# Performance work log

Measured on AMD Instinct MI355X. Metric: run time of the kernel, lower is better.

The kernel has to match this reference:

```python
import jax, jax.numpy as jnp
import numpy as np

EPS = 1e-5

def _layernorm(x, g, b):
    m = jnp.mean(x, axis=-1, keepdims=True)
    v = jnp.mean((x - m) ** 2, axis=-1, keepdims=True)
    return (x - m) * jax.lax.rsqrt(v + EPS) * g + b

def setup_inputs() -> dict:
    key = jax.random.key(0)
    ks = jax.random.split(key, 16)
    B, N, L, E, D, NL = 1, 40962, 256, 4, 163848, 6
    inp = {}
    inp['mesh_latent'] = jax.random.normal(ks[0], (B, N, L), dtype=jnp.float32)
    inp['edge_index'] = jax.random.randint(ks[1], (2, D), 0, N, dtype=jnp.int32)
    inp['edge_attr'] = jax.random.normal(ks[2], (D, E), dtype=jnp.float32)
    s_e = 1.0 / np.sqrt(2 * L + E)
    s_n = 1.0 / np.sqrt(2 * L)
    s_o = 1.0 / np.sqrt(L)
    inp['We_w'] = jax.random.uniform(ks[3], (NL, 2 * L + E, L), jnp.float32, -s_e, s_e)
    inp['We_b'] = jax.random.uniform(ks[4], (NL, L), jnp.float32, -s_e, s_e)
    inp['ln1_g'] = jnp.ones((NL, L), jnp.float32)
    inp['ln1_b'] = jnp.zeros((NL, L), jnp.float32)
    inp['Wn1_w'] = jax.random.uniform(ks[5], (NL, 2 * L, L), jnp.float32, -s_n, s_n)
    inp['Wn1_b'] = jax.random.uniform(ks[6], (NL, L), jnp.float32, -s_n, s_n)
    inp['ln2_g'] = jnp.ones((NL, L), jnp.float32)
    inp['ln2_b'] = jnp.zeros((NL, L), jnp.float32)
    inp['Wn2_w'] = jax.random.uniform(ks[7], (NL, L, L), jnp.float32, -s_o, s_o)
    inp['Wn2_b'] = jax.random.uniform(ks[8], (NL, L), jnp.float32, -s_o, s_o)
    return inp

def reference(mesh_latent, edge_index, edge_attr, We_w, We_b, ln1_g, ln1_b,
              Wn1_w, Wn1_b, ln2_g, ln2_b, Wn2_w, Wn2_b):
    src = edge_index[0]  # x_j (source)
    dst = edge_index[1]  # x_i (target), also aggregation index
    N = mesh_latent.shape[1]
    L = mesh_latent.shape[2]
    # precompute edge_attr contribution is layer-dependent, done inside scan

    def layer(x, p):
        we_w, we_b, g1, b1, wn1_w, wn1_b, g2, b2, wn2_w, wn2_b = p
        x_i = x[dst]  # [E, L] target node feats
        x_j = x[src]  # [E, L] source node feats
        # edge MLP on cat([x_i, x_j, edge_attr]) without materializing the concat
        h = x_i @ we_w[:L] + x_j @ we_w[L:2 * L] + edge_attr @ we_w[2 * L:] + we_b
        msg = jax.nn.silu(_layernorm(h, g1, b1))  # [E, L]
        agg = jax.ops.segment_sum(msg, dst, num_segments=N)  # [N, L]
        u = x @ wn1_w[:L] + agg @ wn1_w[L:] + wn1_b
        u = jax.nn.silu(_layernorm(u, g2, b2)) @ wn2_w + wn2_b
        return x + u, None

    params = (We_w, We_b, ln1_g, ln1_b, Wn1_w, Wn1_b, ln2_g, ln2_b, Wn2_w, Wn2_b)

    def per_sample(x):
        x_out, _ = jax.lax.scan(layer, x, params)
        return x_out

    return jax.vmap(per_sample)(mesh_latent)
```

## Files before the change

### kernel.cpp

```cpp
#include <hip/hip_runtime.h>
#include <hip/hip_bf16.h>
#include <math.h>


#define NNODES 40962
#define NEDGES 163848
#define NLAYERS 6

typedef __attribute__((ext_vector_type(8))) short short8;
typedef __attribute__((ext_vector_type(4))) float f32x4;

__device__ __forceinline__ void async_copy16(void* lds, const void* g) {
    __builtin_amdgcn_global_load_lds(
        (const __attribute__((address_space(1))) unsigned int*)g,
        (__attribute__((address_space(3))) unsigned int*)lds, 16, 0, 0);
}

__global__ __launch_bounds__(256) void wprep_kernel(
    const float* __restrict__ src, unsigned short* __restrict__ dst,
    int R, int C, size_t src_lstride, size_t src_hstride, int halves)
{
    __shared__ float t[32][33];
    const int b = blockIdx.z;
    src += (size_t)(b / halves) * src_lstride + (size_t)(b % halves) * src_hstride;
    dst += (size_t)b * R * C;
    const int tx = threadIdx.x & 31, ty = threadIdx.x >> 5;
    const int c0 = blockIdx.x * 32, r0 = blockIdx.y * 32;
    #pragma unroll
    for (int i = 0; i < 4; ++i)
        t[ty + 8 * i][tx] = src[(size_t)(r0 + ty + 8 * i) * C + c0 + tx];
    __syncthreads();
    #pragma unroll
    for (int i = 0; i < 4; ++i) {
        unsigned int u = __float_as_uint(t[tx][ty + 8 * i]);
        unsigned short h = (unsigned short)((u + 0x7FFFu + ((u >> 16) & 1u)) >> 16);
        dst[(size_t)(c0 + ty + 8 * i) * R + r0 + tx] = h;
    }
}

__global__ __launch_bounds__(256) void gemm_mfma(
    const float* __restrict__ A1, const float* __restrict__ A2,
    const unsigned short* __restrict__ BT,
    const float* __restrict__ bias, const float* __restrict__ resid,
    float* __restrict__ C, int M, int K, int ldC)
{
    __shared__ __align__(16) short Ah[128 * 40];
    __shared__ __align__(16) short Al[128 * 40];
    __shared__ __align__(16) short Bs[128 * 32];

    const int tid = threadIdx.x;
    const int wave = tid >> 6;
    const int lane = tid & 63;
    const int m0 = blockIdx.x * 128;
    const int n0 = blockIdx.y * 128;
    const int wm = wave >> 1;
    const int wn = wave & 1;
    const int fm = lane & 15;
    const int quad = lane >> 4;
    const int ko = quad * 8;

    const int arow = tid >> 1;
    const int akh = (tid & 1) * 16;
    const int gr_stage = m0 + arow;

    f32x4 acc[4][4];
    #pragma unroll
    for (int i = 0; i < 4; ++i)
        #pragma unroll
        for (int j = 0; j < 4; ++j)
            acc[i][j] = (f32x4){0.f, 0.f, 0.f, 0.f};

    const int nkt = K >> 5;
    for (int kt = 0; kt < nkt; ++kt) {
        const int k0 = kt << 5;
        const float* Asrc; int kb;
        if (A2 != nullptr && k0 >= 256) { Asrc = A2; kb = k0 - 256; }
        else                            { Asrc = A1; kb = k0; }

        {
            const int n_row = wave * 32 + (lane >> 2);
            const char* gbase = (const char*)BT + (((size_t)(n0 + n_row) * K + k0) << 1)
                              + ((lane & 3) << 4);
            char* lbase = (char*)Bs + wave * 2048;
            async_copy16(lbase, gbase);
            const char* gbase2 = gbase + ((size_t)16 * K << 1);
            async_copy16(lbase + 1024, gbase2);
        }

        {
            float f[16];
            if (gr_stage < M) {
                const float* ap = Asrc + (size_t)gr_stage * 256 + kb + akh;
                #pragma unroll
                for (int i = 0; i < 4; ++i) {
                    f32x4 v = *(const f32x4*)(ap + 4 * i);
                    f[4 * i + 0] = v.x; f[4 * i + 1] = v.y;
                    f[4 * i + 2] = v.z; f[4 * i + 3] = v.w;
                }
            } else {
                #pragma unroll
                for (int i = 0; i < 16; ++i) f[i] = 0.f;
            }
            unsigned int hid[8], lod[8];
            #pragma unroll
            for (int i = 0; i < 8; ++i) {
                unsigned int u0 = __float_as_uint(f[2 * i]);
                unsigned int u1 = __float_as_uint(f[2 * i + 1]);
                float l0 = f[2 * i]     - __uint_as_float(u0 & 0xFFFF0000u);
                float l1 = f[2 * i + 1] - __uint_as_float(u1 & 0xFFFF0000u);
                hid[i] = (u0 >> 16) | (u1 & 0xFFFF0000u);
                lod[i] = (__float_as_uint(l0) >> 16) | (__float_as_uint(l1) & 0xFFFF0000u);
            }
            short* ah = &Ah[arow * 40 + akh];
            short* al = &Al[arow * 40 + akh];
            ((uint4*)ah)[0] = make_uint4(hid[0], hid[1], hid[2], hid[3]);
            ((uint4*)ah)[1] = make_uint4(hid[4], hid[5], hid[6], hid[7]);
            ((uint4*)al)[0] = make_uint4(lod[0], lod[1], lod[2], lod[3]);
            ((uint4*)al)[1] = make_uint4(lod[4], lod[5], lod[6], lod[7]);
        }

        __syncthreads();

        short8 afh[4], afl[4], bf[4];
        #pragma unroll
        for (int i = 0; i < 4; ++i) {
            const int r = wm * 64 + i * 16 + fm;
            afh[i] = *(const short8*)&Ah[r * 40 + ko];
            afl[i] = *(const short8*)&Al[r * 40 + ko];
        }
        #pragma unroll
        for (int j = 0; j < 4; ++j) {
            const int r = wn * 64 + j * 16 + fm;
            bf[j] = *(const short8*)&Bs[r * 32 + ko];
        }
        #pragma unroll
        for (int i = 0; i < 4; ++i)
            #pragma unroll
            for (int j = 0; j < 4; ++j) {
                acc[i][j] = __builtin_amdgcn_mfma_f32_16x16x32_bf16(afl[i], bf[j], acc[i][j], 0, 0, 0);
                acc[i][j] = __builtin_amdgcn_mfma_f32_16x16x32_bf16(afh[i], bf[j], acc[i][j], 0, 0, 0);
            }

        __syncthreads();
    }

    #pragma unroll
    for (int j = 0; j < 4; ++j) {
        const int gc = n0 + wn * 64 + j * 16 + fm;
        const float bj = bias ? bias[gc] : 0.f;
        #pragma unroll
        for (int i = 0; i < 4; ++i) {
            #pragma unroll
            for (int r = 0; r < 4; ++r) {
                const int gr = m0 + wm * 64 + i * 16 + quad * 4 + r;
                if (gr < M) {
                    float v = acc[i][j][r] + bj;
                    if (resid) v += resid[(size_t)gr * ldC + gc];
                    C[(size_t)gr * ldC + gc] = v;
                }
            }
        }
    }
}

__device__ __forceinline__ float wave_sum(float v) {
    #pragma unroll
    for (int o = 32; o > 0; o >>= 1) v += __shfl_xor(v, o);
    return v;
}

__global__ __launch_bounds__(256) void count_kernel(
    const int* __restrict__ dst, int* __restrict__ deg, int E)
{
    int e = blockIdx.x * 256 + threadIdx.x;
    if (e < E) atomicAdd(&deg[dst[e]], 1);
}

__global__ __launch_bounds__(1024) void scan_kernel(
    const int* __restrict__ deg, int* __restrict__ rowptr, int n)
{
    __shared__ int wsum[16];
    __shared__ int carry_s;
    const int tid = threadIdx.x;
    const int lane = tid & 63, wave = tid >> 6;
    if (tid == 0) carry_s = 0;
    __syncthreads();

    for (int base = 0; base < n; base += 1024) {
        int i = base + tid;
        int v = (i < n) ? deg[i] : 0;
        int x = v;
        #pragma unroll
        for (int o = 1; o < 64; o <<= 1) {
            int t = __shfl_up(x, o);
            if (lane >= o) x += t;
        }
        if (lane == 63) wsum[wave] = x;
        __syncthreads();
        if (wave == 0 && lane < 16) {
            int w = wsum[lane];
            #pragma unroll
            for (int o = 1; o < 16; o <<= 1) {
                int t = __shfl_up(w, o);
                if (lane >= o) w += t;
            }
            wsum[lane] = w;
        }
        __syncthreads();
        int wave_off = (wave == 0) ? 0 : wsum[wave - 1];
        int incl = x + wave_off + carry_s;
        if (i < n) rowptr[i] = incl - v;
        __syncthreads();
        if (tid == 0) carry_s += wsum[15];
        __syncthreads();
    }
    if (tid == 0) rowptr[n] = carry_s;
}

__global__ __launch_bounds__(256) void scatter_kernel(
    const int* __restrict__ dst, int* __restrict__ cursor,
    int* __restrict__ esorted, int E)
{
    int e = blockIdx.x * 256 + threadIdx.x;
    if (e < E) {
        int p = atomicAdd(&cursor[dst[e]], 1);
        esorted[p] = e;
    }
}

__global__ __launch_bounds__(256) void node_agg_kernel(
    const float* __restrict__ P,
    const int* __restrict__ src,
    const float* __restrict__ attr,
    const float* __restrict__ W3,
    const float* __restrict__ be, const float* __restrict__ g1, const float* __restrict__ b1,
    const int* __restrict__ rowptr, const int* __restrict__ esorted,
    float* __restrict__ agg, int N)
{
    const int wave = threadIdx.x >> 6;
    const int lane = threadIdx.x & 63;
    const int n = blockIdx.x * 4 + wave;
    if (n >= N) return;
    const int c0 = lane * 4;

    float4 p1 = *(const float4*)(P + (size_t)n * 512 + c0);
    const float* p1p = (const float*)&p1;

    float w30[4], w31[4], w32[4], w33[4], bev[4], g1v[4], b1v[4];
    #pragma unroll
    for (int i = 0; i < 4; ++i) {
        const int c = c0 + i;
        w30[i] = W3[c]; w31[i] = W3[256 + c]; w32[i] = W3[512 + c]; w33[i] = W3[768 + c];
        bev[i] = be[c]; g1v[i] = g1[c]; b1v[i] = b1[c];
    }

    float acc[4] = {0.f, 0.f, 0.f, 0.f};
    const int beg = rowptr[n];
    const int end = rowptr[n + 1];

    for (int i = beg; i < end; ++i) {
        const int e = esorted[i];
        const int s = src[e];
        float4 ps = *(const float4*)(P + (size_t)s * 512 + 256 + c0);
        const float* psp = (const float*)&ps;
        float4 av = *(const float4*)(attr + (size_t)e * 4);

        float h[4];
        #pragma unroll
        for (int j = 0; j < 4; ++j) {
            float w = av.x * w30[j] + av.y * w31[j] + av.z * w32[j] + av.w * w33[j];
            h[j] = p1p[j] + psp[j] + w + bev[j];
        }

        float sum = wave_sum(h[0] + h[1] + h[2] + h[3]);
        const float mean = sum * (1.0f / 256.0f);
        float vs = 0.f;
        #pragma unroll
        for (int j = 0; j < 4; ++j) { float t = h[j] - mean; vs += t * t; }
        vs = wave_sum(vs);
        const float rstd = rsqrtf(vs * (1.0f / 256.0f) + 1e-5f);

        #pragma unroll
        for (int j = 0; j < 4; ++j) {
            float y = (h[j] - mean) * rstd * g1v[j] + b1v[j];
            acc[j] += y / (1.0f + __expf(-y));
        }
    }

    *(float4*)(agg + (size_t)n * 256 + c0) = make_float4(acc[0], acc[1], acc[2], acc[3]);
}

__global__ __launch_bounds__(256) void ln_silu_kernel(
    float* __restrict__ u, const float* __restrict__ g, const float* __restrict__ b, int N)
{
    const int wave = threadIdx.x >> 6;
    const int lane = threadIdx.x & 63;
    const int r = blockIdx.x * 4 + wave;
    if (r >= N) return;

    float4 hv = *(const float4*)(u + (size_t)r * 256 + lane * 4);
    float h[4] = {hv.x, hv.y, hv.z, hv.w};

    float sum = wave_sum(h[0] + h[1] + h[2] + h[3]);
    const float mean = sum * (1.0f / 256.0f);
    float vs = 0.f;
    #pragma unroll
    for (int i = 0; i < 4; ++i) { float t = h[i] - mean; vs += t * t; }
    vs = wave_sum(vs);
    const float rstd = rsqrtf(vs * (1.0f / 256.0f) + 1e-5f);

    #pragma unroll
    for (int i = 0; i < 4; ++i) {
        const int c = lane * 4 + i;
        float y = (h[i] - mean) * rstd * g[c] + b[c];
        h[i] = y / (1.0f + __expf(-y));
    }
    *(float4*)(u + (size_t)r * 256 + lane * 4) = make_float4(h[0], h[1], h[2], h[3]);
}

extern "C" void kernel_launch(void* const* d_in, const int* in_sizes, int n_in,
                              void* d_out, int out_size, void* d_ws, size_t ws_size,
                              hipStream_t stream) {
    const float* mesh   = (const float*)d_in[0];
    const int*   eidx   = (const int*)  d_in[1];
    const float* eattr  = (const float*)d_in[2];
    const float* We_w   = (const float*)d_in[3];
    const float* We_b   = (const float*)d_in[4];
    const float* ln1_g  = (const float*)d_in[5];
    const float* ln1_b  = (const float*)d_in[6];
    const float* Wn1_w  = (const float*)d_in[7];
    const float* Wn1_b  = (const float*)d_in[8];
    const float* ln2_g  = (const float*)d_in[9];
    const float* ln2_b  = (const float*)d_in[10];
    const float* Wn2_w  = (const float*)d_in[11];
    const float* Wn2_b  = (const float*)d_in[12];

    const int N = NNODES, E = NEDGES;

    float* x   = (float*)d_out;
    float* P   = (float*)d_ws;
    float* u   = P;
    float* agg = P + (size_t)N * 512;
    int*   deg     = (int*)(agg + (size_t)N * 256);
    int*   rowptr  = deg + N;
    int*   cursor  = rowptr + (N + 1);
    int*   esorted = cursor + N;
    uintptr_t wp = (uintptr_t)(esorted + E);
    wp = (wp + 63) & ~(uintptr_t)63;
    unsigned short* BTe  = (unsigned short*)wp;
    unsigned short* BTn1 = BTe  + (size_t)6 * 512 * 256;
    unsigned short* BTn2 = BTn1 + (size_t)6 * 256 * 512;

    const int* src = eidx;
    const int* dst = eidx + E;

    hipMemcpyAsync(x, mesh, (size_t)N * 256 * sizeof(float),
                   hipMemcpyDeviceToDevice, stream);

    wprep_kernel<<<dim3(8, 8, 12), 256, 0, stream>>>(
        We_w, BTe, 256, 256, (size_t)516 * 256, (size_t)256 * 256, 2);
    wprep_kernel<<<dim3(8, 16, 6), 256, 0, stream>>>(
        Wn1_w, BTn1, 512, 256, (size_t)512 * 256, 0, 1);
    wprep_kernel<<<dim3(8, 8, 6), 256, 0, stream>>>(
        Wn2_w, BTn2, 256, 256, (size_t)256 * 256, 0, 1);

    hipMemsetAsync(deg, 0, (size_t)N * sizeof(int), stream);
    count_kernel<<<(E + 255) / 256, 256, 0, stream>>>(dst, deg, E);
    scan_kernel<<<1, 1024, 0, stream>>>(deg, rowptr, N);
    hipMemcpyAsync(cursor, rowptr, (size_t)N * sizeof(int),
                   hipMemcpyDeviceToDevice, stream);
    scatter_kernel<<<(E + 255) / 256, 256, 0, stream>>>(dst, cursor, esorted, E);

    const int mblocks = (N + 127) / 128;
    const int node_blocks = (N + 3) / 4;

    for (int l = 0; l < NLAYERS; ++l) {
        const float* W3  = We_w + (size_t)l * 516 * 256 + (size_t)512 * 256;
        const float* be  = We_b  + (size_t)l * 256;
        const float* g1  = ln1_g + (size_t)l * 256;
        const float* b1  = ln1_b + (size_t)l * 256;
        const float* bn1 = Wn1_b + (size_t)l * 256;
        const float* g2  = ln2_g + (size_t)l * 256;
        const float* b2  = ln2_b + (size_t)l * 256;
        const float* bn2 = Wn2_b + (size_t)l * 256;
        const unsigned short* bte  = BTe  + (size_t)l * 512 * 256;
        const unsigned short* btn1 = BTn1 + (size_t)l * 256 * 512;
        const unsigned short* btn2 = BTn2 + (size_t)l * 256 * 256;

        gemm_mfma<<<dim3(mblocks, 4), 256, 0, stream>>>(
            x, nullptr, bte, nullptr, nullptr, P, N, 256, 512);
        node_agg_kernel<<<node_blocks, 256, 0, stream>>>(
            P, src, eattr, W3, be, g1, b1, rowptr, esorted, agg, N);
        gemm_mfma<<<dim3(mblocks, 2), 256, 0, stream>>>(
            x, agg, btn1, bn1, nullptr, u, N, 512, 256);
        ln_silu_kernel<<<node_blocks, 256, 0, stream>>>(u, g2, b2, N);
        gemm_mfma<<<dim3(mblocks, 2), 256, 0, stream>>>(
            u, nullptr, btn2, bn2, x, x, N, 256, 256);
    }
}
```

Before: 1.519 ms.

## Pre-split activations to bf16 hi/lo in producers and async-load A tiles

Producers (split kernel, node aggregation, LN-SiLU, and the residual GEMM epilogue) now write activations as separate bf16 high and low halves. The GEMM can then stream A tiles with global_load_lds through an XOR-swizzled LDS layout instead of loading fp32 and converting in registers. Rows are padded to a multiple of 128 with zeroed tails so no bounds checks are needed. Node aggregation also processes two edges per iteration with prefetching, and both LayerNorms use a single-pass sum and sum-of-squares reduction, which risks some precision loss.

```diff
diff --git a/kernel.cpp b/kernel.cpp
--- a/kernel.cpp
+++ b/kernel.cpp
@@ -6,9 +6,11 @@
 #define NNODES 40962
 #define NEDGES 163848
 #define NLAYERS 6
+#define MPAD 41088
 
 typedef __attribute__((ext_vector_type(8))) short short8;
 typedef __attribute__((ext_vector_type(4))) float f32x4;
+typedef unsigned short ushort_t;
 
 __device__ __forceinline__ void async_copy16(void* lds, const void* g) {
     __builtin_amdgcn_global_load_lds(
@@ -16,8 +18,15 @@
         (__attribute__((address_space(3))) unsigned int*)lds, 16, 0, 0);
 }
 
+__device__ __forceinline__ void bsplit(float v, ushort_t& h, ushort_t& l) {
+    unsigned int u = __float_as_uint(v);
+    h = (ushort_t)(u >> 16);
+    float hf = __uint_as_float(u & 0xFFFF0000u);
+    l = (ushort_t)(__float_as_uint(v - hf) >> 16);
+}
+
 __global__ __launch_bounds__(256) void wprep_kernel(
-    const float* __restrict__ src, unsigned short* __restrict__ dst,
+    const float* __restrict__ src, ushort_t* __restrict__ dst,
     int R, int C, size_t src_lstride, size_t src_hstride, int halves)
 {
     __shared__ float t[32][33];
@@ -33,35 +42,54 @@
     #pragma unroll
     for (int i = 0; i < 4; ++i) {
         unsigned int u = __float_as_uint(t[tx][ty + 8 * i]);
-        unsigned short h = (unsigned short)((u + 0x7FFFu + ((u >> 16) & 1u)) >> 16);
+        ushort_t h = (ushort_t)((u + 0x7FFFu + ((u >> 16) & 1u)) >> 16);
         dst[(size_t)(c0 + ty + 8 * i) * R + r0 + tx] = h;
     }
 }
 
+__global__ __launch_bounds__(256) void split_kernel(
+    const float* __restrict__ x, ushort_t* __restrict__ xh,
+    ushort_t* __restrict__ xl, int n4)
+{
+    int idx = blockIdx.x * 256 + threadIdx.x;
+    if (idx >= n4) return;
+    float4 v = ((const float4*)x)[idx];
+    ushort4 oh, ol;
+    bsplit(v.x, oh.x, ol.x); bsplit(v.y, oh.y, ol.y);
+    bsplit(v.z, oh.z, ol.z); bsplit(v.w, oh.w, ol.w);
+    ((ushort4*)xh)[idx] = oh;
+    ((ushort4*)xl)[idx] = ol;
+}
+
 __global__ __launch_bounds__(256) void gemm_mfma(
-    const float* __restrict__ A1, const float* __restrict__ A2,
-    const unsigned short* __restrict__ BT,
+    const ushort_t* __restrict__ A1h, const ushort_t* __restrict__ A1l,
+    const ushort_t* __restrict__ A2h, const ushort_t* __restrict__ A2l,
+    const ushort_t* __restrict__ BT,
     const float* __restrict__ bias, const float* __restrict__ resid,
-    float* __restrict__ C, int M, int K, int ldC)
-{
-    __shared__ __align__(16) short Ah[128 * 40];
-    __shared__ __align__(16) short Al[128 * 40];
-    __shared__ __align__(16) short Bs[128 * 32];
+    float* __restrict__ C, ushort_t* __restrict__ Ch, ushort_t* __restrict__ Cl,
+    int M, int K, int ldC)
+{
+    __shared__ __align__(16) short AhS[128 * 32];
+    __shared__ __align__(16) short AlS[128 * 32];
+    __shared__ __align__(16) short BsS[128 * 32];
 
     const int tid = threadIdx.x;
     const int wave = tid >> 6;
     const int lane = tid & 63;
     const int m0 = blockIdx.x * 128;
     const int n0 = blockIdx.y * 128;
-    const int wm = wave >> 1;
-    const int wn = wave & 1;
-    const int fm = lane & 15;
-    const int quad = lane >> 4;
-    const int ko = quad * 8;
-
-    const int arow = tid >> 1;
-    const int akh = (tid & 1) * 16;
-    const int gr_stage = m0 + arow;
+    const int wm = wave >> 1, wn = wave & 1;
+    const int fm = lane & 15, quad = lane >> 4;
+
+    const int rA = wave * 32 + (lane >> 2);
+    const int qg = (lane & 3) ^ ((lane >> 3) & 3);
+    const size_t offA = (size_t)(m0 + rA) * 256 + qg * 8;
+    const size_t offB = (size_t)(n0 + rA) * (size_t)K + qg * 8;
+    char* ldsAh = (char*)AhS + wave * 2048;
+    char* ldsAl = (char*)AlS + wave * 2048;
+    char* ldsB  = (char*)BsS + wave * 2048;
+
+    const int sq16 = ((quad ^ ((fm >> 1) & 3)) << 4);
 
     f32x4 acc[4][4];
     #pragma unroll
@@ -73,51 +101,17 @@
     const int nkt = K >> 5;
     for (int kt = 0; kt < nkt; ++kt) {
         const int k0 = kt << 5;
-        const float* Asrc; int kb;
-        if (A2 != nullptr && k0 >= 256) { Asrc = A2; kb = k0 - 256; }
-        else                            { Asrc = A1; kb = k0; }
-
-        {
-            const int n_row = wave * 32 + (lane >> 2);
-            const char* gbase = (const char*)BT + (((size_t)(n0 + n_row) * K + k0) << 1)
-                              + ((lane & 3) << 4);
-            char* lbase = (char*)Bs + wave * 2048;
-            async_copy16(lbase, gbase);
-            const char* gbase2 = gbase + ((size_t)16 * K << 1);
-            async_copy16(lbase + 1024, gbase2);
-        }
-
-        {
-            float f[16];
-            if (gr_stage < M) {
-                const float* ap = Asrc + (size_t)gr_stage * 256 + kb + akh;
-                #pragma unroll
-                for (int i = 0; i < 4; ++i) {
-                    f32x4 v = *(const f32x4*)(ap + 4 * i);
-                    f[4 * i + 0] = v.x; f[4 * i + 1] = v.y;
-                    f[4 * i + 2] = v.z; f[4 * i + 3] = v.w;
-                }
-            } else {
-                #pragma unroll
-                for (int i = 0; i < 16; ++i) f[i] = 0.f;
-            }
-            unsigned int hid[8], lod[8];
-            #pragma unroll
-            for (int i = 0; i < 8; ++i) {
-                unsigned int u0 = __float_as_uint(f[2 * i]);
-                unsigned int u1 = __float_as_uint(f[2 * i + 1]);
-                float l0 = f[2 * i]     - __uint_as_float(u0 & 0xFFFF0000u);
-                float l1 = f[2 * i + 1] - __uint_as_float(u1 & 0xFFFF0000u);
-                hid[i] = (u0 >> 16) | (u1 & 0xFFFF0000u);
-                lod[i] = (__float_as_uint(l0) >> 16) | (__float_as_uint(l1) & 0xFFFF0000u);
-            }
-            short* ah = &Ah[arow * 40 + akh];
-            short* al = &Al[arow * 40 + akh];
-            ((uint4*)ah)[0] = make_uint4(hid[0], hid[1], hid[2], hid[3]);
-            ((uint4*)ah)[1] = make_uint4(hid[4], hid[5], hid[6], hid[7]);
-            ((uint4*)al)[0] = make_uint4(lod[0], lod[1], lod[2], lod[3]);
-            ((uint4*)al)[1] = make_uint4(lod[4], lod[5], lod[6], lod[7]);
-        }
+        const ushort_t* Ah_g = A1h;
+        const ushort_t* Al_g = A1l;
+        int kb = k0;
+        if (k0 >= 256) { Ah_g = A2h; Al_g = A2l; kb = k0 - 256; }
+
+        async_copy16(ldsAh,        Ah_g + offA + kb);
+        async_copy16(ldsAh + 1024, Ah_g + offA + 4096 + kb);
+        async_copy16(ldsAl,        Al_g + offA + kb);
+        async_copy16(ldsAl + 1024, Al_g + offA + 4096 + kb);
+        async_copy16(ldsB,         BT + offB + k0);
+        async_copy16(ldsB + 1024,  BT + offB + (size_t)16 * K + k0);
 
         __syncthreads();
 
@@ -125,13 +119,13 @@
         #pragma unroll
         for (int i = 0; i < 4; ++i) {
             const int r = wm * 64 + i * 16 + fm;
-            afh[i] = *(const short8*)&Ah[r * 40 + ko];
-            afl[i] = *(const short8*)&Al[r * 40 + ko];
+            afh[i] = *(const short8*)((const char*)AhS + (r << 6) + sq16);
+            afl[i] = *(const short8*)((const char*)AlS + (r << 6) + sq16);
         }
         #pragma unroll
         for (int j = 0; j < 4; ++j) {
             const int r = wn * 64 + j * 16 + fm;
-            bf[j] = *(const short8*)&Bs[r * 32 + ko];
+            bf[j] = *(const short8*)((const char*)BsS + (r << 6) + sq16);
         }
         #pragma unroll
         for (int i = 0; i < 4; ++i)
@@ -157,6 +151,12 @@
                     float v = acc[i][j][r] + bj;
                     if (resid) v += resid[(size_t)gr * ldC + gc];
                     C[(size_t)gr * ldC + gc] = v;
+                    if (Ch) {
+                        ushort_t hs, ls;
+                        bsplit(v, hs, ls);
+                        Ch[(size_t)gr * 256 + gc] = hs;
+                        Cl[(size_t)gr * 256 + gc] = ls;
+                    }
                 }
             }
         }
@@ -235,7 +235,7 @@
     const float* __restrict__ W3,
     const float* __restrict__ be, const float* __restrict__ g1, const float* __restrict__ b1,
     const int* __restrict__ rowptr, const int* __restrict__ esorted,
-    float* __restrict__ agg, int N)
+    ushort_t* __restrict__ aggh, ushort_t* __restrict__ aggl, int N)
 {
     const int wave = threadIdx.x >> 6;
     const int lane = threadIdx.x & 63;
@@ -258,40 +258,77 @@
     const int beg = rowptr[n];
     const int end = rowptr[n + 1];
 
-    for (int i = beg; i < end; ++i) {
-        const int e = esorted[i];
-        const int s = src[e];
-        float4 ps = *(const float4*)(P + (size_t)s * 512 + 256 + c0);
-        const float* psp = (const float*)&ps;
-        float4 av = *(const float4*)(attr + (size_t)e * 4);
-
-        float h[4];
-        #pragma unroll
-        for (int j = 0; j < 4; ++j) {
-            float w = av.x * w30[j] + av.y * w31[j] + av.z * w32[j] + av.w * w33[j];
-            h[j] = p1p[j] + psp[j] + w + bev[j];
-        }
-
-        float sum = wave_sum(h[0] + h[1] + h[2] + h[3]);
-        const float mean = sum * (1.0f / 256.0f);
-        float vs = 0.f;
-        #pragma unroll
-        for (int j = 0; j < 4; ++j) { float t = h[j] - mean; vs += t * t; }
-        vs = wave_sum(vs);
-        const float rstd = rsqrtf(vs * (1.0f / 256.0f) + 1e-5f);
-
-        #pragma unroll
-        for (int j = 0; j < 4; ++j) {
-            float y = (h[j] - mean) * rstd * g1v[j] + b1v[j];
-            acc[j] += y / (1.0f + __expf(-y));
-        }
-    }
-
-    *(float4*)(agg + (size_t)n * 256 + c0) = make_float4(acc[0], acc[1], acc[2], acc[3]);
+    if (beg < end) {
+        int iB0 = (beg + 1 < end) ? beg + 1 : beg;
+        int eA = esorted[beg], eB = esorted[iB0];
+        int sA = src[eA], sB = src[eB];
+        float4 psA = *(const float4*)(P + (size_t)sA * 512 + 256 + c0);
+        float4 avA = *(const float4*)(attr + (size_t)eA * 4);
+        float4 psB = *(const float4*)(P + (size_t)sB * 512 + 256 + c0);
+        float4 avB = *(const float4*)(attr + (size_t)eB * 4);
+        bool vB = (beg + 1 < end);
+
+        for (int i = beg; i < end; i += 2) {
+            int jA = (i + 2 < end) ? i + 2 : i;
+            int jB = (i + 3 < end) ? i + 3 : jA;
+            int eA2 = esorted[jA], eB2 = esorted[jB];
+            int sA2 = src[eA2], sB2 = src[eB2];
+            float4 psA2 = *(const float4*)(P + (size_t)sA2 * 512 + 256 + c0);
+            float4 avA2 = *(const float4*)(attr + (size_t)eA2 * 4);
+            float4 psB2 = *(const float4*)(P + (size_t)sB2 * 512 + 256 + c0);
+            float4 avB2 = *(const float4*)(attr + (size_t)eB2 * 4);
+
+            const float* pA = (const float*)&psA;
+            const float* pB = (const float*)&psB;
+            float hA[4], hB[4];
+            #pragma unroll
+            for (int j = 0; j < 4; ++j) {
+                float wA = avA.x * w30[j] + avA.y * w31[j] + avA.z * w32[j] + avA.w * w33[j];
+                hA[j] = p1p[j] + pA[j] + wA + bev[j];
+                float wB = avB.x * w30[j] + avB.y * w31[j] + avB.z * w32[j] + avB.w * w33[j];
+                hB[j] = p1p[j] + pB[j] + wB + bev[j];
+            }
+
+            float s1A = hA[0] + hA[1] + hA[2] + hA[3];
+            float s2A = hA[0]*hA[0] + hA[1]*hA[1] + hA[2]*hA[2] + hA[3]*hA[3];
+            float s1B = hB[0] + hB[1] + hB[2] + hB[3];
+            float s2B = hB[0]*hB[0] + hB[1]*hB[1] + hB[2]*hB[2] + hB[3]*hB[3];
+            #pragma unroll
+            for (int o = 32; o > 0; o >>= 1) {
+                s1A += __shfl_xor(s1A, o); s2A += __shfl_xor(s2A, o);
+                s1B += __shfl_xor(s1B, o); s2B += __shfl_xor(s2B, o);
+            }
+            const float mA = s1A * (1.0f / 256.0f);
+            const float vrA = fmaxf(s2A * (1.0f / 256.0f) - mA * mA, 0.f);
+            const float rA = rsqrtf(vrA + 1e-5f);
+            const float mB = s1B * (1.0f / 256.0f);
+            const float vrB = fmaxf(s2B * (1.0f / 256.0f) - mB * mB, 0.f);
+            const float rB = rsqrtf(vrB + 1e-5f);
+            const float addB = vB ? 1.f : 0.f;
+
+            #pragma unroll
+            for (int j = 0; j < 4; ++j) {
+                float yA = (hA[j] - mA) * rA * g1v[j] + b1v[j];
+                acc[j] += yA / (1.0f + __expf(-yA));
+                float yB = (hB[j] - mB) * rB * g1v[j] + b1v[j];
+                acc[j] += addB * (yB / (1.0f + __expf(-yB)));
+            }
+
+            psA = psA2; avA = avA2; psB = psB2; avB = avB2;
+            vB = (i + 3 < end);
+        }
+    }
+
+    ushort4 oh, ol;
+    bsplit(acc[0], oh.x, ol.x); bsplit(acc[1], oh.y, ol.y);
+    bsplit(acc[2], oh.z, ol.z); bsplit(acc[3], oh.w, ol.w);
+    *(ushort4*)(aggh + (size_t)n * 256 + c0) = oh;
+    *(ushort4*)(aggl + (size_t)n * 256 + c0) = ol;
 }
 
 __global__ __launch_bounds__(256) void ln_silu_kernel(
-    float* __restrict__ u, const float* __restrict__ g, const float* __restrict__ b, int N)
+    const float* __restrict__ u, const float* __restrict__ g, const float* __restrict__ b,
+    ushort_t* __restrict__ sh, ushort_t* __restrict__ sl, int N)
 {
     const int wave = threadIdx.x >> 6;
     const int lane = threadIdx.x & 63;
@@ -301,21 +338,27 @@
     float4 hv = *(const float4*)(u + (size_t)r * 256 + lane * 4);
     float h[4] = {hv.x, hv.y, hv.z, hv.w};
 
-    float sum = wave_sum(h[0] + h[1] + h[2] + h[3]);
-    const float mean = sum * (1.0f / 256.0f);
-    float vs = 0.f;
-    #pragma unroll
-    for (int i = 0; i < 4; ++i) { float t = h[i] - mean; vs += t * t; }
-    vs = wave_sum(vs);
-    const float rstd = rsqrtf(vs * (1.0f / 256.0f) + 1e-5f);
-
+    float s1 = h[0] + h[1] + h[2] + h[3];
+    float s2 = h[0]*h[0] + h[1]*h[1] + h[2]*h[2] + h[3]*h[3];
+    #pragma unroll
+    for (int o = 32; o > 0; o >>= 1) {
+        s1 += __shfl_xor(s1, o); s2 += __shfl_xor(s2, o);
+    }
+    const float mean = s1 * (1.0f / 256.0f);
+    const float var = fmaxf(s2 * (1.0f / 256.0f) - mean * mean, 0.f);
+    const float rstd = rsqrtf(var + 1e-5f);
+
+    ushort4 oh, ol;
     #pragma unroll
     for (int i = 0; i < 4; ++i) {
         const int c = lane * 4 + i;
         float y = (h[i] - mean) * rstd * g[c] + b[c];
         h[i] = y / (1.0f + __expf(-y));
     }
-    *(float4*)(u + (size_t)r * 256 + lane * 4) = make_float4(h[0], h[1], h[2], h[3]);
+    bsplit(h[0], oh.x, ol.x); bsplit(h[1], oh.y, ol.y);
+    bsplit(h[2], oh.z, ol.z); bsplit(h[3], oh.w, ol.w);
+    *(ushort4*)(sh + (size_t)r * 256 + lane * 4) = oh;
+    *(ushort4*)(sl + (size_t)r * 256 + lane * 4) = ol;
 }
 
 extern "C" void kernel_launch(void* const* d_in, const int* in_sizes, int n_in,
@@ -337,25 +380,38 @@
 
     const int N = NNODES, E = NEDGES;
 
-    float* x   = (float*)d_out;
-    float* P   = (float*)d_ws;
-    float* u   = P;
-    float* agg = P + (size_t)N * 512;
-    int*   deg     = (int*)(agg + (size_t)N * 256);
+    float* x = (float*)d_out;
+    float* P = (float*)d_ws;
+    float* u = P;
+    int*   deg     = (int*)(P + (size_t)N * 512);
     int*   rowptr  = deg + N;
     int*   cursor  = rowptr + (N + 1);
     int*   esorted = cursor + N;
     uintptr_t wp = (uintptr_t)(esorted + E);
     wp = (wp + 63) & ~(uintptr_t)63;
-    unsigned short* BTe  = (unsigned short*)wp;
-    unsigned short* BTn1 = BTe  + (size_t)6 * 512 * 256;
-    unsigned short* BTn2 = BTn1 + (size_t)6 * 256 * 512;
+    ushort_t* BTe  = (ushort_t*)wp;
+    ushort_t* BTn1 = BTe  + (size_t)6 * 512 * 256;
+    ushort_t* BTn2 = BTn1 + (size_t)6 * 256 * 512;
+    ushort_t* xh   = BTn2 + (size_t)6 * 256 * 256;
+    ushort_t* xl   = xh + (size_t)MPAD * 256;
+    ushort_t* sh   = xl + (size_t)MPAD * 256;
+    ushort_t* sl   = sh + (size_t)MPAD * 256;
 
     const int* src = eidx;
     const int* dst = eidx + E;
 
     hipMemcpyAsync(x, mesh, (size_t)N * 256 * sizeof(float),
                    hipMemcpyDeviceToDevice, stream);
+
+    const size_t padoff = (size_t)N * 256;
+    const size_t padbytes = (size_t)(MPAD - N) * 256 * sizeof(ushort_t);
+    hipMemsetAsync(xh + padoff, 0, padbytes, stream);
+    hipMemsetAsync(xl + padoff, 0, padbytes, stream);
+    hipMemsetAsync(sh + padoff, 0, padbytes, stream);
+    hipMemsetAsync(sl + padoff, 0, padbytes, stream);
+
+    const int n4 = N * 64;
+    split_kernel<<<(n4 + 255) / 256, 256, 0, stream>>>(mesh, xh, xl, n4);
 
     wprep_kernel<<<dim3(8, 8, 12), 256, 0, stream>>>(
         We_w, BTe, 256, 256, (size_t)516 * 256, (size_t)256 * 256, 2);
@@ -371,7 +427,7 @@
                    hipMemcpyDeviceToDevice, stream);
     scatter_kernel<<<(E + 255) / 256, 256, 0, stream>>>(dst, cursor, esorted, E);
 
-    const int mblocks = (N + 127) / 128;
+    const int mblocks = MPAD / 128;
     const int node_blocks = (N + 3) / 4;
 
     for (int l = 0; l < NLAYERS; ++l) {
@@ -383,18 +439,22 @@
         const float* g2  = ln2_g + (size_t)l * 256;
         const float* b2  = ln2_b + (size_t)l * 256;
         const float* bn2 = Wn2_b + (size_t)l * 256;
-        const unsigned short* bte  = BTe  + (size_t)l * 512 * 256;
-        const unsigned short* btn1 = BTn1 + (size_t)l * 256 * 512;
-        const unsigned short* btn2 = BTn2 + (size_t)l * 256 * 256;
+        const ushort_t* bte  = BTe  + (size_t)l * 512 * 256;
+        const ushort_t* btn1 = BTn1 + (size_t)l * 256 * 512;
+        const ushort_t* btn2 = BTn2 + (size_t)l * 256 * 256;
 
         gemm_mfma<<<dim3(mblocks, 4), 256, 0, stream>>>(
-            x, nullptr, bte, nullptr, nullptr, P, N, 256, 512);
+            xh, xl, nullptr, nullptr, bte, nullptr, nullptr,
+            P, nullptr, nullptr, N, 256, 512);
         node_agg_kernel<<<node_blocks, 256, 0, stream>>>(
-            P, src, eattr, W3, be, g1, b1, rowptr, esorted, agg, N);
+            P, src, eattr, W3, be, g1, b1, rowptr, esorted, sh, sl, N);
         gemm_mfma<<<dim3(mblocks, 2), 256, 0, stream>>>(
-            x, agg, btn1, bn1, nullptr, u, N, 512, 256);
-        ln_silu_kernel<<<node_blocks, 256, 0, stream>>>(u, g2, b2, N);
+            xh, xl, sh, sl, btn1, bn1, nullptr,
+            u, nullptr, nullptr, N, 512, 256);
+        ln_silu_kernel<<<node_blocks, 256, 0, stream>>>(u, g2, b2, sh, sl, N);
         gemm_mfma<<<dim3(mblocks, 2), 256, 0, stream>>>(
-            u, nullptr, btn2, bn2, x, x, N, 256, 256);
-    }
-}
+            sh, sl, nullptr, nullptr, btn2, bn2, x,
+            x, (l < NLAYERS - 1) ? xh : nullptr, (l < NLAYERS - 1) ? xl : nullptr,
+            N, 256, 256);
+    }
+}
```

After: 1.791 ms. +17.8%, slower.
